# Kernel optimization log

Measured on AMD Instinct MI355X. Metric: run time of the kernel, lower is better.

Reference implementation:

```python
import jax, jax.numpy as jnp
import numpy as np

N_NODES = 20000
BN_EPS = 1e-5


def setup_inputs() -> dict:
    key = jax.random.key(0)
    ks = jax.random.split(key, 8)
    in_dim, half, out_dim, n_edges = 256, 128, 256, 320000
    s = 1.0 / np.sqrt(in_dim)
    return {
        "x": jax.random.normal(ks[0], (N_NODES, in_dim), dtype=jnp.float32),
        "edge_index": jax.random.randint(ks[1], (2, n_edges), 0, N_NODES, dtype=jnp.int64),
        "W_l_f": jax.random.normal(ks[2], (half, in_dim), dtype=jnp.float32) * s,
        "b_l_f": jnp.zeros((half,), dtype=jnp.float32),
        "W_r_f": jax.random.normal(ks[3], (half, in_dim), dtype=jnp.float32) * s,
        "W_l_b": jax.random.normal(ks[4], (half, in_dim), dtype=jnp.float32) * s,
        "b_l_b": jnp.zeros((half,), dtype=jnp.float32),
        "W_r_b": jax.random.normal(ks[5], (half, in_dim), dtype=jnp.float32) * s,
        "gamma": jnp.ones((out_dim,), dtype=jnp.float32),
        "beta": jnp.zeros((out_dim,), dtype=jnp.float32),
    }


def _sage(x, src, dst, W_l, b_l, W_r):
    # mean-aggregate source features at destination nodes (PyG SAGEConv, aggr='mean')
    msg_sum = jax.ops.segment_sum(x[src], dst, num_segments=N_NODES)
    cnt = jax.ops.segment_sum(jnp.ones((src.shape[0],), x.dtype), dst, num_segments=N_NODES)
    aggr = msg_sum / jnp.maximum(cnt, 1.0)[:, None]
    # lin_l(aggr) + lin_r(x); lin_l carries the bias in PyG
    return aggr @ W_l.T + b_l + x @ W_r.T


def reference(x, edge_index, W_l_f, b_l_f, W_r_f, W_l_b, b_l_b, W_r_b, gamma, beta):
    src, dst = edge_index[0], edge_index[1]
    h_fwd = _sage(x, src, dst, W_l_f, b_l_f, W_r_f)
    h_bwd = _sage(x, dst, src, W_l_b, b_l_b, W_r_b)  # flipped edges
    h = jnp.concatenate([h_fwd, h_bwd], axis=-1)  # [N, out_dim]
    # BatchNorm1d in training mode (N > 1), biased variance
    mean = jnp.mean(h, axis=0)
    var = jnp.mean(jnp.square(h - mean), axis=0)
    h = (h - mean) * jax.lax.rsqrt(var + BN_EPS) * gamma + beta
    return jax.nn.relu(h)
```

## Files before the change

kernel.cpp:

```cpp
#include <hip/hip_runtime.h>
#include <hip/hip_bf16.h>

#define N_NODES 20000
#define N_EDGES 320000
#define BN_EPS  1e-5f

#define FILL_BLK ((N_EDGES + 255) / 256)
#define GEMM_MT  ((N_NODES + 127) / 128)

typedef __attribute__((ext_vector_type(4))) float f32x4;
typedef __attribute__((ext_vector_type(8))) __bf16 bf16x8;
typedef __attribute__((ext_vector_type(4))) unsigned short u16x4;

__device__ __forceinline__ unsigned short f2bf(float f) {
    unsigned int u = __float_as_uint(f);
    u += 0x7fffu + ((u >> 16) & 1u);
    return (unsigned short)(u >> 16);
}
__device__ __forceinline__ float bflo(unsigned int u) { return __uint_as_float(u << 16); }
__device__ __forceinline__ float bfhi(unsigned int u) { return __uint_as_float(u & 0xffff0000u); }

__device__ __forceinline__ void gload_lds16(const void* g, void* l) {
    __builtin_amdgcn_global_load_lds(
        (const __attribute__((address_space(1))) void*)g,
        (__attribute__((address_space(3))) void*)l, 16, 0, 0);
}

__global__ __launch_bounds__(256) void cvt_zero_kernel(
    const float* __restrict__ x,
    const float* __restrict__ Wlf, const float* __restrict__ Wlb,
    const float* __restrict__ Wrf, const float* __restrict__ Wrb,
    unsigned short* __restrict__ Xb, unsigned short* __restrict__ Wb,
    uint4* __restrict__ zp, int zquads)
{
    const int XQ = N_NODES * 256 / 4;
    const int WQ = 128 * 256 / 4;
    const int total = XQ + 4 * WQ + zquads;
    for (int i = blockIdx.x * blockDim.x + threadIdx.x; i < total; i += gridDim.x * blockDim.x) {
        if (i >= XQ + 4 * WQ) {
            zp[i - XQ - 4 * WQ] = make_uint4(0, 0, 0, 0);
            continue;
        }
        const float* sp;
        unsigned short* dp;
        if (i < XQ) {
            sp = x + (size_t)i * 4;
            dp = Xb + (size_t)i * 4;
        } else {
            int w = i - XQ;
            int mat = w / WQ;
            int o = (w - mat * WQ) * 4;
            if      (mat == 0) sp = Wlf + o;
            else if (mat == 1) sp = Wlb + o;
            else if (mat == 2) sp = Wrf + o;
            else               sp = Wrb + o;
            dp = Wb + (size_t)mat * 32768 + o;
        }
        float4 v = *(const float4*)sp;
        u16x4 r = {f2bf(v.x), f2bf(v.y), f2bf(v.z), f2bf(v.w)};
        *(u16x4*)dp = r;
    }
}

__global__ void count_kernel(const int* __restrict__ src, const int* __restrict__ dst,
                             int* __restrict__ cntF, int* __restrict__ cntB) {
    int e = blockIdx.x * blockDim.x + threadIdx.x;
    if (e < N_EDGES) {
        atomicAdd(&cntF[dst[e]], 1);
        atomicAdd(&cntB[src[e]], 1);
    }
}

#define SCAN_PER 20
__global__ __launch_bounds__(1024) void scan_kernel(const int* __restrict__ cntF, int* __restrict__ offF,
                                                    const int* __restrict__ cntB, int* __restrict__ offB) {
    const int* in  = blockIdx.x ? cntB : cntF;
    int*       out = blockIdx.x ? offB : offF;
    int t = threadIdx.x;
    int base = t * SCAN_PER;
    int v[SCAN_PER];
    int sum = 0;
    #pragma unroll
    for (int k = 0; k < SCAN_PER; ++k) {
        int i = base + k;
        int c = (i < N_NODES) ? in[i] : 0;
        v[k] = sum; sum += c;
    }
    __shared__ int sh[1024];
    sh[t] = sum;
    __syncthreads();
    for (int o = 1; o < 1024; o <<= 1) {
        int x = (t >= o) ? sh[t - o] : 0;
        __syncthreads();
        sh[t] += x;
        __syncthreads();
    }
    int pre = t ? sh[t - 1] : 0;
    #pragma unroll
    for (int k = 0; k < SCAN_PER; ++k) {
        int i = base + k;
        if (i < N_NODES) out[i] = pre + v[k];
    }
    if (t == 1023) out[N_NODES] = sh[1023];
}

__global__ __launch_bounds__(256) void fill_gemm_kernel(
    const int* __restrict__ src, const int* __restrict__ dst,
    const int* __restrict__ offF, const int* __restrict__ offB,
    int* __restrict__ curF, int* __restrict__ curB,
    int* __restrict__ listF, int* __restrict__ listB,
    const unsigned short* __restrict__ Xb, const unsigned short* __restrict__ Wb,
    unsigned short* __restrict__ Y, float* __restrict__ Z)
{
    __shared__ unsigned short As[128 * 64];
    __shared__ unsigned short Bs[128 * 64];

    if (blockIdx.x < FILL_BLK) {
        int e = blockIdx.x * blockDim.x + threadIdx.x;
        if (e < N_EDGES) {
            int s = src[e], d = dst[e];
            int p = atomicAdd(&curF[d], 1);
            listF[offF[d] + p] = s;
            int q = atomicAdd(&curB[s], 1);
            listB[offB[s] + q] = d;
        }
        return;
    }

    int gb = blockIdx.x - FILL_BLK;
    int by = gb & 3;
    int mBase = (gb >> 2) * 128;
    int tid = threadIdx.x, lane = tid & 63, wave = tid >> 6;
    int wr = wave >> 1, wc = wave & 1;
    const unsigned short* W = Wb + (size_t)by * 128 * 256;

    f32x4 acc[4][4] = {};

    for (int k0 = 0; k0 < 256; k0 += 64) {
        #pragma unroll
        for (int c = 0; c < 4; ++c) {
            int S = c * 256 + tid;
            int row = S >> 3;
            int q = (S & 7) ^ (row & 7);
            int gm = mBase + row; gm = gm < N_NODES ? gm : N_NODES - 1;
            gload_lds16(Xb + (size_t)gm * 256 + k0 + q * 8, &As[S * 8]);
            gload_lds16(W + (size_t)row * 256 + k0 + q * 8, &Bs[S * 8]);
        }
        asm volatile("s_waitcnt vmcnt(0)" ::: "memory");
        __syncthreads();

        #pragma unroll
        for (int ks = 0; ks < 2; ++ks) {
            bf16x8 af[4], bfr[4];
            int sl = ks * 4 + (lane >> 4);
            #pragma unroll
            for (int m = 0; m < 4; ++m) {
                int row = wr * 64 + m * 16 + (lane & 15);
                af[m] = *(const bf16x8*)&As[row * 64 + ((sl ^ (row & 7)) * 8)];
            }
            #pragma unroll
            for (int n = 0; n < 4; ++n) {
                int row = wc * 64 + n * 16 + (lane & 15);
                bfr[n] = *(const bf16x8*)&Bs[row * 64 + ((sl ^ (row & 7)) * 8)];
            }
            #pragma unroll
            for (int m = 0; m < 4; ++m)
                #pragma unroll
                for (int n = 0; n < 4; ++n)
                    acc[m][n] = __builtin_amdgcn_mfma_f32_16x16x32_bf16(af[m], bfr[n], acc[m][n], 0, 0, 0);
        }
        __syncthreads();
    }

    bool toY = by < 2;
    int cBase = (by & 1) * 128 + wc * 64;
    #pragma unroll
    for (int m = 0; m < 4; ++m) {
        int gm0 = mBase + wr * 64 + m * 16 + (lane >> 4) * 4;
        #pragma unroll
        for (int n = 0; n < 4; ++n) {
            int gn = cBase + n * 16 + (lane & 15);
            f32x4 v = acc[m][n];
            #pragma unroll
            for (int j = 0; j < 4; ++j) {
                int gm = gm0 + j;
                if (gm < N_NODES) {
                    if (toY) Y[(size_t)gm * 256 + gn] = f2bf(v[j]);
                    else     Z[(size_t)gm * 256 + gn] = v[j];
                }
            }
        }
    }
}

#define NPW 2
__global__ __launch_bounds__(256) void aggregate_kernel(
    const unsigned short* __restrict__ Y,
    const int* __restrict__ offF, const int* __restrict__ listF,
    const int* __restrict__ offB, const int* __restrict__ listB,
    float* __restrict__ H)
{
    int tid = threadIdx.x, lane = tid & 63, wave = tid >> 6;
    int dir = wave >> 1, half = wave & 1;
    const int* off  = dir ? offB : offF;
    const int* list = dir ? listB : listF;
    int eg = lane >> 4;
    int c16 = lane & 15;
    int nodeBase = blockIdx.x * (2 * NPW) + half * NPW;

    for (int jn = 0; jn < NPW; ++jn) {
        int n = nodeBase + jn;
        int beg = off[n], end = off[n + 1];
        int deg = end - beg;
        float acc[8] = {0.f, 0.f, 0.f, 0.f, 0.f, 0.f, 0.f, 0.f};

        for (int i = beg; i < end; i += 64) {
            int c = end - i; if (c > 64) c = 64;
            int u_l = list[i + (lane < c ? lane : 0)];
            for (int e0 = 0; e0 < c; e0 += 16) {
                uint4 v[4];
                #pragma unroll
                for (int k = 0; k < 4; ++k) {
                    int ei = e0 + k * 4 + eg;
                    int u = __shfl(u_l, ei < c ? ei : 0);
                    v[k] = make_uint4(0u, 0u, 0u, 0u);
                    if (ei < c)
                        v[k] = *(const uint4*)(Y + (size_t)u * 256 + dir * 128 + c16 * 8);
                }
                #pragma unroll
                for (int k = 0; k < 4; ++k) {
                    acc[0] += bflo(v[k].x); acc[1] += bfhi(v[k].x);
                    acc[2] += bflo(v[k].y); acc[3] += bfhi(v[k].y);
                    acc[4] += bflo(v[k].z); acc[5] += bfhi(v[k].z);
                    acc[6] += bflo(v[k].w); acc[7] += bfhi(v[k].w);
                }
            }
        }
        #pragma unroll
        for (int j = 0; j < 8; ++j) {
            acc[j] += __shfl_xor(acc[j], 16);
            acc[j] += __shfl_xor(acc[j], 32);
        }
        float h0 = (eg & 2) ? ((eg & 1) ? acc[6] : acc[4]) : ((eg & 1) ? acc[2] : acc[0]);
        float h1 = (eg & 2) ? ((eg & 1) ? acc[7] : acc[5]) : ((eg & 1) ? acc[3] : acc[1]);
        float inv = 1.f / fmaxf((float)deg, 1.f);
        float2* hp = (float2*)(H + (size_t)n * 256 + dir * 128 + c16 * 8 + eg * 2);
        float2 z = *hp;
        *hp = make_float2(fmaf(h0, inv, z.x), fmaf(h1, inv, z.y));
    }
}

__global__ __launch_bounds__(256) void bn_stats_kernel(const float* __restrict__ H,
                                                       float* __restrict__ stats) {
    int col = threadIdx.x;
    float s1 = 0.f, s2 = 0.f;
    for (int n = blockIdx.x; n < N_NODES; n += gridDim.x) {
        float h = H[(size_t)n * 256 + col];
        s1 += h;
        s2 += h * h;
    }
    atomicAdd(&stats[col], s1);
    atomicAdd(&stats[256 + col], s2);
}

__global__ __launch_bounds__(256) void bn_kernel(
    const float* __restrict__ stats, const float* __restrict__ gamma,
    const float* __restrict__ beta, float* __restrict__ H)
{
    __shared__ float sc[256], sf[256];
    int tid = threadIdx.x;
    {
        float mean = stats[tid] * (1.f / N_NODES);
        float var  = stats[256 + tid] * (1.f / N_NODES) - mean * mean;
        float s = rsqrtf(fmaxf(var, 0.f) + BN_EPS) * gamma[tid];
        sc[tid] = s;
        sf[tid] = beta[tid] - mean * s;
    }
    __syncthreads();
    for (int n = blockIdx.x; n < N_NODES; n += gridDim.x) {
        size_t idx = (size_t)n * 256 + tid;
        float h = H[idx];
        H[idx] = fmaxf(h * sc[tid] + sf[tid], 0.f);
    }
}

extern "C" void kernel_launch(void* const* d_in, const int* in_sizes, int n_in,
                              void* d_out, int out_size, void* d_ws, size_t ws_size,
                              hipStream_t stream) {
    const float* x     = (const float*)d_in[0];
    const int*   edge  = (const int*)d_in[1];
    const float* Wlf   = (const float*)d_in[2];
    const float* Wrf   = (const float*)d_in[4];
    const float* Wlb   = (const float*)d_in[5];
    const float* Wrb   = (const float*)d_in[7];
    const float* gamma = (const float*)d_in[8];
    const float* beta  = (const float*)d_in[9];
    float* out = (float*)d_out;

    const int* src = edge;
    const int* dst = edge + N_EDGES;

    char* ws = (char*)d_ws;
    size_t off = 0;
    auto alloc = [&](size_t bytes) { size_t r = off; off += (bytes + 255) & ~(size_t)255; return r; };
    unsigned short* Y  = (unsigned short*)(ws + alloc((size_t)N_NODES * 256 * 2));
    unsigned short* Xb = (unsigned short*)(ws + alloc((size_t)N_NODES * 256 * 2));
    unsigned short* Wb = (unsigned short*)(ws + alloc((size_t)4 * 128 * 256 * 2));
    int* offF  = (int*)(ws + alloc((size_t)(N_NODES + 1) * 4));
    int* offB  = (int*)(ws + alloc((size_t)(N_NODES + 1) * 4));
    int* listF = (int*)(ws + alloc((size_t)N_EDGES * 4));
    int* listB = (int*)(ws + alloc((size_t)N_EDGES * 4));
    size_t zbase_off = off;
    int* cntF = (int*)(ws + alloc((size_t)N_NODES * 4));
    int* cntB = (int*)(ws + alloc((size_t)N_NODES * 4));
    int* curF = (int*)(ws + alloc((size_t)N_NODES * 4));
    int* curB = (int*)(ws + alloc((size_t)N_NODES * 4));
    float* stats = (float*)(ws + alloc(512 * 4));
    size_t zbytes = off - zbase_off;

    cvt_zero_kernel<<<2048, 256, 0, stream>>>(x, Wlf, Wlb, Wrf, Wrb, Xb, Wb,
                                              (uint4*)(ws + zbase_off), (int)(zbytes / 16));

    count_kernel<<<FILL_BLK, 256, 0, stream>>>(src, dst, cntF, cntB);
    scan_kernel<<<2, 1024, 0, stream>>>(cntF, offF, cntB, offB);

    fill_gemm_kernel<<<FILL_BLK + GEMM_MT * 4, 256, 0, stream>>>(
        src, dst, offF, offB, curF, curB, listF, listB, Xb, Wb, Y, out);

    aggregate_kernel<<<N_NODES / (2 * NPW), 256, 0, stream>>>(
        Y, offF, listF, offB, listB, out);

    bn_stats_kernel<<<512, 256, 0, stream>>>(out, stats);
    bn_kernel<<<2048, 256, 0, stream>>>(stats, gamma, beta, out);
}
```

Before: 150.9 us.

## Double-buffer GEMM LDS tiles and reorder fused fill blocks after GEMM

The GEMM K-loop now uses two LDS buffers, prefetching the next 64-wide K slice while MFMAs run on the current one, with partial vmcnt waits in place of a full drain each step. The kernel's block order is flipped so GEMM blocks are scheduled first. The edge-fill work moves into 256 grid-stride blocks instead of one block per 256 edges. LDS use doubles to 64KB per block, which may lower occupancy.

```diff
diff --git a/kernel.cpp b/kernel.cpp
--- a/kernel.cpp
+++ b/kernel.cpp
@@ -5,8 +5,9 @@
 #define N_EDGES 320000
 #define BN_EPS  1e-5f
 
-#define FILL_BLK ((N_EDGES + 255) / 256)
 #define GEMM_MT  ((N_NODES + 127) / 128)
+#define NGEMM    (GEMM_MT * 4)
+#define FILLB    256
 
 typedef __attribute__((ext_vector_type(4))) float f32x4;
 typedef __attribute__((ext_vector_type(8))) __bf16 bf16x8;
@@ -104,7 +105,7 @@
     if (t == 1023) out[N_NODES] = sh[1023];
 }
 
-__global__ __launch_bounds__(256) void fill_gemm_kernel(
+__global__ __launch_bounds__(256) void gemm_fill_kernel(
     const int* __restrict__ src, const int* __restrict__ dst,
     const int* __restrict__ offF, const int* __restrict__ offB,
     int* __restrict__ curF, int* __restrict__ curB,
@@ -112,12 +113,11 @@
     const unsigned short* __restrict__ Xb, const unsigned short* __restrict__ Wb,
     unsigned short* __restrict__ Y, float* __restrict__ Z)
 {
-    __shared__ unsigned short As[128 * 64];
-    __shared__ unsigned short Bs[128 * 64];
-
-    if (blockIdx.x < FILL_BLK) {
-        int e = blockIdx.x * blockDim.x + threadIdx.x;
-        if (e < N_EDGES) {
+    __shared__ unsigned short As[2][128 * 64];
+    __shared__ unsigned short Bs[2][128 * 64];
+
+    if (blockIdx.x >= NGEMM) {
+        for (int e = (blockIdx.x - NGEMM) * 256 + threadIdx.x; e < N_EDGES; e += FILLB * 256) {
             int s = src[e], d = dst[e];
             int p = atomicAdd(&curF[d], 1);
             listF[offF[d] + p] = s;
@@ -127,7 +127,7 @@
         return;
     }
 
-    int gb = blockIdx.x - FILL_BLK;
+    int gb = blockIdx.x;
     int by = gb & 3;
     int mBase = (gb >> 2) * 128;
     int tid = threadIdx.x, lane = tid & 63, wave = tid >> 6;
@@ -136,19 +136,18 @@
 
     f32x4 acc[4][4] = {};
 
-    for (int k0 = 0; k0 < 256; k0 += 64) {
+    auto STAGE = [&](int b, int k0) {
         #pragma unroll
         for (int c = 0; c < 4; ++c) {
             int S = c * 256 + tid;
             int row = S >> 3;
             int q = (S & 7) ^ (row & 7);
             int gm = mBase + row; gm = gm < N_NODES ? gm : N_NODES - 1;
-            gload_lds16(Xb + (size_t)gm * 256 + k0 + q * 8, &As[S * 8]);
-            gload_lds16(W + (size_t)row * 256 + k0 + q * 8, &Bs[S * 8]);
-        }
-        asm volatile("s_waitcnt vmcnt(0)" ::: "memory");
-        __syncthreads();
-
+            gload_lds16(Xb + (size_t)gm * 256 + k0 + q * 8, &As[b][S * 8]);
+            gload_lds16(W + (size_t)row * 256 + k0 + q * 8, &Bs[b][S * 8]);
+        }
+    };
+    auto COMPUTE = [&](int b) {
         #pragma unroll
         for (int ks = 0; ks < 2; ++ks) {
             bf16x8 af[4], bfr[4];
@@ -156,12 +155,12 @@
             #pragma unroll
             for (int m = 0; m < 4; ++m) {
                 int row = wr * 64 + m * 16 + (lane & 15);
-                af[m] = *(const bf16x8*)&As[row * 64 + ((sl ^ (row & 7)) * 8)];
+                af[m] = *(const bf16x8*)&As[b][row * 64 + ((sl ^ (row & 7)) * 8)];
             }
             #pragma unroll
             for (int n = 0; n < 4; ++n) {
                 int row = wc * 64 + n * 16 + (lane & 15);
-                bfr[n] = *(const bf16x8*)&Bs[row * 64 + ((sl ^ (row & 7)) * 8)];
+                bfr[n] = *(const bf16x8*)&Bs[b][row * 64 + ((sl ^ (row & 7)) * 8)];
             }
             #pragma unroll
             for (int m = 0; m < 4; ++m)
@@ -169,7 +168,21 @@
                 for (int n = 0; n < 4; ++n)
                     acc[m][n] = __builtin_amdgcn_mfma_f32_16x16x32_bf16(af[m], bfr[n], acc[m][n], 0, 0, 0);
         }
-        __syncthreads();
+    };
+
+    STAGE(0, 0);
+    #pragma unroll
+    for (int t = 0; t < 4; ++t) {
+        if (t < 3) {
+            STAGE((t + 1) & 1, (t + 1) * 64);
+            asm volatile("s_waitcnt vmcnt(8)" ::: "memory");
+        } else {
+            asm volatile("s_waitcnt vmcnt(0)" ::: "memory");
+        }
+        __builtin_amdgcn_s_barrier();
+        __builtin_amdgcn_sched_barrier(0);
+        COMPUTE(t & 1);
+        __builtin_amdgcn_s_barrier();
     }
 
     bool toY = by < 2;
@@ -321,10 +334,10 @@
     cvt_zero_kernel<<<2048, 256, 0, stream>>>(x, Wlf, Wlb, Wrf, Wrb, Xb, Wb,
                                               (uint4*)(ws + zbase_off), (int)(zbytes / 16));
 
-    count_kernel<<<FILL_BLK, 256, 0, stream>>>(src, dst, cntF, cntB);
+    count_kernel<<<(N_EDGES + 255) / 256, 256, 0, stream>>>(src, dst, cntF, cntB);
     scan_kernel<<<2, 1024, 0, stream>>>(cntF, offF, cntB, offB);
 
-    fill_gemm_kernel<<<FILL_BLK + GEMM_MT * 4, 256, 0, stream>>>(
+    gemm_fill_kernel<<<NGEMM + FILLB, 256, 0, stream>>>(
         src, dst, offF, offB, curF, curB, listF, listB, Xb, Wb, Y, out);
 
     aggregate_kernel<<<N_NODES / (2 * NPW), 256, 0, stream>>>(
```

Result: no change. 151.7 us (+0.5%).
